# Optimization experiments

Hardware: AMD Instinct MI355X
Metric: run time of the kernel (lower is better)

## Reference

```python
import jax, jax.numpy as jnp
import numpy as np

B, QL, H, HKV, D, MAX_SEQ = 16, 32, 32, 8, 128, 8192
CACHE_LEN = 4064  # tokens already in cache before this step
SCALE = 1.0 / np.sqrt(D).astype(np.float32)


def setup_inputs() -> dict:
    key = jax.random.key(0)
    ks = jax.random.split(key, 5)
    return {
        "q": jax.random.normal(ks[0], (B, QL, H, D), jnp.float32),
        "k": jax.random.normal(ks[1], (B, QL, HKV, D), jnp.float32),
        "v": jax.random.normal(ks[2], (B, QL, HKV, D), jnp.float32),
        "k_cache": jax.random.normal(ks[3], (B, MAX_SEQ, HKV, D), jnp.float32),
        "v_cache": jax.random.normal(ks[4], (B, MAX_SEQ, HKV, D), jnp.float32),
        "cache_seq_len": CACHE_LEN,
    }


def _attention(q, k_full, v_full):
    # q: [B, QL, H, D]; k_full/v_full: [B, KV, HKV, D]. GQA via head grouping
    # (equivalent to repeat_interleave on kv heads, without materializing it).
    rep = H // HKV
    kv_len = k_full.shape[1]
    qr = q.reshape(B, QL, HKV, rep, D)
    scores = jnp.einsum('bqhrd,bkhd->bhrqk', qr, k_full) * SCALE
    # causal mask: position j masked for query i when j > kv_len - QL + i
    mask = jnp.triu(jnp.ones((QL, kv_len), bool), k=kv_len - QL + 1)
    scores = jnp.where(mask, -jnp.inf, scores)
    weights = jax.nn.softmax(scores, axis=-1)
    out = jnp.einsum('bhrqk,bkhd->bqhrd', weights, v_full)
    return out.reshape(B, QL, H, D)


def reference(q, k, v, k_cache, v_cache, cache_seq_len):
    new_len = cache_seq_len + QL  # python int -> static slice
    k_cache = jax.lax.dynamic_update_slice(k_cache, k, (0, cache_seq_len, 0, 0))
    v_cache = jax.lax.dynamic_update_slice(v_cache, v, (0, cache_seq_len, 0, 0))
    k_full = k_cache[:, :new_len]
    v_full = v_cache[:, :new_len]
    return _attention(q, k_full, v_full)
```

## Files before the change

### kernel.cpp

```cpp
#include <hip/hip_runtime.h>

typedef unsigned short ushort_t;
typedef ushort_t ushort8 __attribute__((ext_vector_type(8)));
typedef __bf16 bf16x8 __attribute__((ext_vector_type(8)));
typedef float f32x4 __attribute__((ext_vector_type(4)));
typedef float f32x16 __attribute__((ext_vector_type(16)));
typedef unsigned uint4v __attribute__((ext_vector_type(4)));

#define B_      16
#define QL_     32
#define H_      32
#define HKV_    8
#define D_      128
#define MAXSEQ_ 8192
#define REP_    4
#define ROWS_   128
#define KT_     64
#define NT_     256
#define KS_LD   136
#define VT_LD   72
#define NROWS_TOT (B_*HKV_*ROWS_)
#define KVSTRIDE (HKV_*D_)

__device__ __forceinline__ unsigned pkbf(float lo, float hi2) {
  unsigned a  = (unsigned)__builtin_bit_cast(ushort_t, (__bf16)lo);
  unsigned b2 = (unsigned)__builtin_bit_cast(ushort_t, (__bf16)hi2);
  return a | (b2 << 16);
}

template<int NSPLIT, bool DIRECT>
__global__ __launch_bounds__(NT_, 2)
void fa_main(const float* __restrict__ qg, const float* __restrict__ kg,
             const float* __restrict__ vg, const float* __restrict__ kcg,
             const float* __restrict__ vcg, const int* __restrict__ cslp,
             float* __restrict__ outg, float* __restrict__ opart,
             float* __restrict__ mpart, float* __restrict__ lpart)
{
  __shared__ __align__(16) ushort_t Ks[2][KT_ * KS_LD];
  __shared__ __align__(16) ushort_t Vt[2][D_ * VT_LD];

  const int t    = threadIdx.x;
  const int s    = (int)blockIdx.x % NSPLIT;
  const int bh   = (int)blockIdx.x / NSPLIT;
  const int b    = bh / HKV_;
  const int h    = bh % HKV_;
  const int cl   = cslp[0];
  const int kvlen = cl + QL_;
  const int ntiles = (kvlen + KT_ - 1) / KT_;
  const int tps  = (ntiles + NSPLIT - 1) / NSPLIT;
  const int tt0  = s * tps;
  const int tt1  = min(ntiles, tt0 + tps);

  const int lane = t & 63;
  const int w    = t >> 6;
  const int qcol = lane & 31;
  const int hi   = lane >> 5;

  const float qscale = 0.088388347648318447f * 1.4426950408889634f;
  bf16x8 aQ[8];
  {
    const float* src = qg + (((size_t)b*QL_ + qcol)*H_ + h*REP_ + w)*D_ + hi*8;
    #pragma unroll
    for (int ks = 0; ks < 8; ++ks) {
      f32x4 v0 = *(const f32x4*)(src + ks*16);
      f32x4 v1 = *(const f32x4*)(src + ks*16 + 4);
      bf16x8 u;
      u[0]=(__bf16)(v0[0]*qscale); u[1]=(__bf16)(v0[1]*qscale);
      u[2]=(__bf16)(v0[2]*qscale); u[3]=(__bf16)(v0[3]*qscale);
      u[4]=(__bf16)(v1[0]*qscale); u[5]=(__bf16)(v1[1]*qscale);
      u[6]=(__bf16)(v1[2]*qscale); u[7]=(__bf16)(v1[3]*qscale);
      aQ[ks] = u;
    }
  }

  f32x16 oacc[4];
  #pragma unroll
  for (int db = 0; db < 4; ++db)
    #pragma unroll
    for (int r = 0; r < 16; ++r) oacc[db][r] = 0.f;
  float m_run = -INFINITY;
  float l_run = 0.f;

  const int k_kl = t >> 2;
  const int k_d0 = (t & 3) * 32;
  const int v_k2 = (t & 31) * 2;
  const int v_d0 = (t >> 5) * 16;

  const float* kc_base = kcg + (size_t)b*MAXSEQ_*KVSTRIDE + h*D_ + k_d0;
  const float* kn_base = kg  + (size_t)b*QL_*KVSTRIDE    + h*D_ + k_d0;
  const float* vc_base = vcg + (size_t)b*MAXSEQ_*KVSTRIDE + h*D_ + v_d0;
  const float* vn_base = vg  + (size_t)b*QL_*KVSTRIDE    + h*D_ + v_d0;

  f32x4 kr[8], vr[8];

  auto issue = [&](int tt) {
    const int p0 = tt * KT_;
    {
      int p = p0 + k_kl; if (p > kvlen - 1) p = kvlen - 1;
      const float* src = (p < cl) ? kc_base + (size_t)p*KVSTRIDE
                                  : kn_base + (size_t)(p - cl)*KVSTRIDE;
      #pragma unroll
      for (int j = 0; j < 8; ++j) kr[j] = *(const f32x4*)(src + 4*j);
    }
    #pragma unroll
    for (int kk = 0; kk < 2; ++kk) {
      int p = p0 + v_k2 + kk; if (p > kvlen - 1) p = kvlen - 1;
      const float* src = (p < cl) ? vc_base + (size_t)p*KVSTRIDE
                                  : vn_base + (size_t)(p - cl)*KVSTRIDE;
      #pragma unroll
      for (int j = 0; j < 4; ++j) vr[kk*4 + j] = *(const f32x4*)(src + 4*j);
    }
  };

  auto commit = [&](int bufi) {
    #pragma unroll
    for (int c2 = 0; c2 < 4; ++c2) {
      ushort8 u;
      #pragma unroll
      for (int e = 0; e < 4; ++e) {
        u[e]   = __builtin_bit_cast(ushort_t, (__bf16)kr[c2*2][e]);
        u[4+e] = __builtin_bit_cast(ushort_t, (__bf16)kr[c2*2+1][e]);
      }
      *(ushort8*)&Ks[bufi][k_kl*KS_LD + k_d0 + c2*8] = u;
    }
    #pragma unroll
    for (int dj = 0; dj < 16; ++dj) {
      const unsigned pr = pkbf(vr[dj>>2][dj&3], vr[4 + (dj>>2)][dj&3]);
      *(unsigned*)&Vt[bufi][(v_d0 + dj)*VT_LD + v_k2] = pr;
    }
  };

  if (tt0 < tt1) { issue(tt0); commit(0); }
  __syncthreads();

  for (int tt = tt0; tt < tt1; ++tt) {
    const int  cur     = (tt - tt0) & 1;
    const bool hasNext = (tt + 1 < tt1);
    if (hasNext) issue(tt + 1);

    const int p0 = tt * KT_;

    f32x16 sacc[2];
    __builtin_amdgcn_s_setprio(1);
    #pragma unroll
    for (int kg = 0; kg < 2; ++kg) {
      #pragma unroll
      for (int r = 0; r < 16; ++r) sacc[kg][r] = 0.f;
      #pragma unroll
      for (int ks = 0; ks < 8; ++ks) {
        bf16x8 ak = __builtin_bit_cast(bf16x8,
            *(const ushort8*)&Ks[cur][(kg*32 + qcol)*KS_LD + ks*16 + hi*8]);
        sacc[kg] = __builtin_amdgcn_mfma_f32_32x32x16_bf16(ak, aQ[ks], sacc[kg], 0, 0, 0);
      }
    }
    __builtin_amdgcn_s_setprio(0);

    if (p0 + KT_ - 1 > cl) {
      #pragma unroll
      for (int kg = 0; kg < 2; ++kg)
        #pragma unroll
        for (int r = 0; r < 16; ++r) {
          const int key = p0 + kg*32 + (r&3) + 8*(r>>2) + 4*hi;
          if (key > cl + qcol) sacc[kg][r] = -INFINITY;
        }
    }

    float tm = -INFINITY;
    #pragma unroll
    for (int kg = 0; kg < 2; ++kg)
      #pragma unroll
      for (int r = 0; r < 16; ++r) tm = fmaxf(tm, sacc[kg][r]);
    tm = fmaxf(tm, __shfl_xor(tm, 32, 64));

    if (__any(tm > m_run + 11.5f)) {
      const float mn    = fmaxf(m_run, tm);
      const float alpha = exp2f(m_run - mn);
      m_run = mn;
      l_run *= alpha;
      #pragma unroll
      for (int r = 0; r < 16; ++r) {
        const int rq = (r&3) + 8*(r>>2) + 4*hi;
        const float ar = __shfl(alpha, rq, 64);
        #pragma unroll
        for (int db = 0; db < 4; ++db) oacc[db][r] *= ar;
      }
    }

    float rs = 0.f;
    #pragma unroll
    for (int kg = 0; kg < 2; ++kg)
      #pragma unroll
      for (int r = 0; r < 16; ++r) {
        const float e = exp2f(sacc[kg][r] - m_run);
        sacc[kg][r] = e;
        rs += e;
      }
    rs += __shfl_xor(rs, 32, 64);
    l_run += rs;

    #pragma unroll
    for (int kg = 0; kg < 2; ++kg) {
      #pragma unroll
      for (int hl = 0; hl < 2; ++hl) {
        const int rb = hl * 8;
        unsigned a0 = pkbf(sacc[kg][rb+0], sacc[kg][rb+1]);
        unsigned b0 = pkbf(sacc[kg][rb+4], sacc[kg][rb+5]);
        unsigned a1 = pkbf(sacc[kg][rb+2], sacc[kg][rb+3]);
        unsigned b1 = pkbf(sacc[kg][rb+6], sacc[kg][rb+7]);
        asm volatile("v_permlane32_swap_b32 %0, %1" : "+v"(a0), "+v"(b0));
        asm volatile("v_permlane32_swap_b32 %0, %1" : "+v"(a1), "+v"(b1));
        uint4v wv; wv[0] = a0; wv[1] = a1; wv[2] = b0; wv[3] = b1;
        const bf16x8 ap = __builtin_bit_cast(bf16x8, wv);
        const int kbase = kg*32 + hl*16;
        __builtin_amdgcn_s_setprio(1);
        #pragma unroll
        for (int db = 0; db < 4; ++db) {
          bf16x8 bv = __builtin_bit_cast(bf16x8,
              *(const ushort8*)&Vt[cur][(db*32 + qcol)*VT_LD + kbase + hi*8]);
          oacc[db] = __builtin_amdgcn_mfma_f32_32x32x16_bf16(ap, bv, oacc[db], 0, 0, 0);
        }
        __builtin_amdgcn_s_setprio(0);
      }
    }

    if (hasNext) commit(cur ^ 1);
    __syncthreads();
  }

  const float inv_own = (l_run > 0.f) ? 1.f / l_run : 0.f;
  if constexpr (DIRECT) {
    #pragma unroll
    for (int r = 0; r < 16; ++r) {
      const int rq = (r&3) + 8*(r>>2) + 4*hi;
      const float inv = __shfl(inv_own, rq, 64);
      float* dst = outg + (((size_t)b*QL_ + rq)*H_ + h*REP_ + w)*D_ + qcol;
      #pragma unroll
      for (int db = 0; db < 4; ++db) dst[db*32] = oacc[db][r] * inv;
    }
  } else {
    const int R0 = bh * ROWS_ + w * 32;
    #pragma unroll
    for (int r = 0; r < 16; ++r) {
      const int rq = (r&3) + 8*(r>>2) + 4*hi;
      float* dst = opart + ((size_t)s*NROWS_TOT + R0 + rq)*D_ + qcol;
      #pragma unroll
      for (int db = 0; db < 4; ++db) dst[db*32] = oacc[db][r];
    }
    if (lane < 32) {
      mpart[s*NROWS_TOT + R0 + lane] = m_run;
      lpart[s*NROWS_TOT + R0 + lane] = l_run;
    }
  }
}

template<int NS>
__global__ void fa_combine(const float* __restrict__ opart,
                           const float* __restrict__ mpart,
                           const float* __restrict__ lpart,
                           float* __restrict__ outg)
{
  const int idx = (int)blockIdx.x * 256 + (int)threadIdx.x;
  const int R = idx >> 7;
  const int d = idx & 127;
  float mm = -INFINITY;
  #pragma unroll
  for (int si = 0; si < NS; ++si) mm = fmaxf(mm, mpart[si*NROWS_TOT + R]);
  float L = 0.f, o = 0.f;
  #pragma unroll
  for (int si = 0; si < NS; ++si) {
    const float ms = mpart[si*NROWS_TOT + R];
    const float wgt = (ms == -INFINITY) ? 0.f : exp2f(ms - mm);
    L += lpart[si*NROWS_TOT + R] * wgt;
    o += opart[((size_t)si*NROWS_TOT + R)*D_ + d] * wgt;
  }
  const float res = (L > 0.f) ? o / L : 0.f;
  const int b   = R >> 10;
  const int h   = (R >> 7) & 7;
  const int row = R & 127;
  outg[(((size_t)b*QL_ + (row & 31))*H_ + h*REP_ + (row >> 5))*D_ + d] = res;
}

extern "C" void kernel_launch(void* const* d_in, const int* in_sizes, int n_in,
                              void* d_out, int out_size, void* d_ws, size_t ws_size,
                              hipStream_t stream)
{
  const float* qg  = (const float*)d_in[0];
  const float* kg  = (const float*)d_in[1];
  const float* vg  = (const float*)d_in[2];
  const float* kcg = (const float*)d_in[3];
  const float* vcg = (const float*)d_in[4];
  const int*   csl = (const int*)d_in[5];
  float* outg = (float*)d_out;

  const size_t need4 = (size_t)4 * NROWS_TOT * (D_ + 2) * sizeof(float);
  const size_t need2 = (size_t)2 * NROWS_TOT * (D_ + 2) * sizeof(float);
  if (ws_size >= need4) {
    float* opart = (float*)d_ws;
    float* mpart = opart + (size_t)4 * NROWS_TOT * D_;
    float* lpart = mpart + 4 * NROWS_TOT;
    hipLaunchKernelGGL((fa_main<4, false>), dim3(4 * B_ * HKV_), dim3(NT_), 0, stream,
                       qg, kg, vg, kcg, vcg, csl, nullptr, opart, mpart, lpart);
    hipLaunchKernelGGL((fa_combine<4>), dim3(NROWS_TOT * D_ / 256), dim3(256), 0, stream,
                       opart, mpart, lpart, outg);
  } else if (ws_size >= need2) {
    float* opart = (float*)d_ws;
    float* mpart = opart + (size_t)2 * NROWS_TOT * D_;
    float* lpart = mpart + 2 * NROWS_TOT;
    hipLaunchKernelGGL((fa_main<2, false>), dim3(2 * B_ * HKV_), dim3(NT_), 0, stream,
                       qg, kg, vg, kcg, vcg, csl, nullptr, opart, mpart, lpart);
    hipLaunchKernelGGL((fa_combine<2>), dim3(NROWS_TOT * D_ / 256), dim3(256), 0, stream,
                       opart, mpart, lpart, outg);
  } else {
    hipLaunchKernelGGL((fa_main<1, true>), dim3(B_ * HKV_), dim3(NT_), 0, stream,
                       qg, kg, vg, kcg, vcg, csl, outg, nullptr, nullptr, nullptr);
  }
}
```

Measured before the change: 130.1 us.

## Fuse split-KV combine into main kernel via last-block atomic counter

Removes the separate combine kernel. Each split block writes its partials, then increments a per-(batch,head) atomic counter, and the last arriving block merges all splits and writes the output with vectorized loads and stores. It also remaps block indices so that consecutive blocks with the same batch share the same KV head, which may improve L2 locality of K/V reads. The cost is a memset launch for the counters, threadfences, and a serialized tail merge done by one block per group.

```diff
diff --git a/kernel.cpp b/kernel.cpp
--- a/kernel.cpp
+++ b/kernel.cpp
@@ -34,16 +34,29 @@
              const float* __restrict__ vg, const float* __restrict__ kcg,
              const float* __restrict__ vcg, const int* __restrict__ cslp,
              float* __restrict__ outg, float* __restrict__ opart,
-             float* __restrict__ mpart, float* __restrict__ lpart)
+             float* __restrict__ mpart, float* __restrict__ lpart,
+             int* __restrict__ ctrs)
 {
   __shared__ __align__(16) ushort_t Ks[2][KT_ * KS_LD];
   __shared__ __align__(16) ushort_t Vt[2][D_ * VT_LD];
-
-  const int t    = threadIdx.x;
-  const int s    = (int)blockIdx.x % NSPLIT;
-  const int bh   = (int)blockIdx.x / NSPLIT;
-  const int b    = bh / HKV_;
-  const int h    = bh % HKV_;
+  __shared__ int lastFlag;
+
+  const int t = threadIdx.x;
+  int b, h, s;
+  if constexpr (NSPLIT == 4) {
+    const int nid = (int)blockIdx.x;
+    const int g   = ((nid >> 6) << 3) | (nid & 7);
+    h = (nid >> 3) & 7;
+    b = g >> 2;
+    s = g & 3;
+  } else {
+    s = (int)blockIdx.x % NSPLIT;
+    const int bh0 = (int)blockIdx.x / NSPLIT;
+    b = bh0 / HKV_;
+    h = bh0 % HKV_;
+  }
+  const int bh = b * HKV_ + h;
+
   const int cl   = cslp[0];
   const int kvlen = cl + QL_;
   const int ntiles = (kvlen + KT_ - 1) / KT_;
@@ -143,33 +156,33 @@
     f32x16 sacc[2];
     __builtin_amdgcn_s_setprio(1);
     #pragma unroll
-    for (int kg = 0; kg < 2; ++kg) {
-      #pragma unroll
-      for (int r = 0; r < 16; ++r) sacc[kg][r] = 0.f;
+    for (int kg2 = 0; kg2 < 2; ++kg2) {
+      #pragma unroll
+      for (int r = 0; r < 16; ++r) sacc[kg2][r] = 0.f;
       #pragma unroll
       for (int ks = 0; ks < 8; ++ks) {
         bf16x8 ak = __builtin_bit_cast(bf16x8,
-            *(const ushort8*)&Ks[cur][(kg*32 + qcol)*KS_LD + ks*16 + hi*8]);
-        sacc[kg] = __builtin_amdgcn_mfma_f32_32x32x16_bf16(ak, aQ[ks], sacc[kg], 0, 0, 0);
+            *(const ushort8*)&Ks[cur][(kg2*32 + qcol)*KS_LD + ks*16 + hi*8]);
+        sacc[kg2] = __builtin_amdgcn_mfma_f32_32x32x16_bf16(ak, aQ[ks], sacc[kg2], 0, 0, 0);
       }
     }
     __builtin_amdgcn_s_setprio(0);
 
     if (p0 + KT_ - 1 > cl) {
       #pragma unroll
-      for (int kg = 0; kg < 2; ++kg)
+      for (int kg2 = 0; kg2 < 2; ++kg2)
         #pragma unroll
         for (int r = 0; r < 16; ++r) {
-          const int key = p0 + kg*32 + (r&3) + 8*(r>>2) + 4*hi;
-          if (key > cl + qcol) sacc[kg][r] = -INFINITY;
+          const int key = p0 + kg2*32 + (r&3) + 8*(r>>2) + 4*hi;
+          if (key > cl + qcol) sacc[kg2][r] = -INFINITY;
         }
     }
 
     float tm = -INFINITY;
     #pragma unroll
-    for (int kg = 0; kg < 2; ++kg)
-      #pragma unroll
-      for (int r = 0; r < 16; ++r) tm = fmaxf(tm, sacc[kg][r]);
+    for (int kg2 = 0; kg2 < 2; ++kg2)
+      #pragma unroll
+      for (int r = 0; r < 16; ++r) tm = fmaxf(tm, sacc[kg2][r]);
     tm = fmaxf(tm, __shfl_xor(tm, 32, 64));
 
     if (__any(tm > m_run + 11.5f)) {
@@ -188,30 +201,30 @@
 
     float rs = 0.f;
     #pragma unroll
-    for (int kg = 0; kg < 2; ++kg)
+    for (int kg2 = 0; kg2 < 2; ++kg2)
       #pragma unroll
       for (int r = 0; r < 16; ++r) {
-        const float e = exp2f(sacc[kg][r] - m_run);
-        sacc[kg][r] = e;
+        const float e = exp2f(sacc[kg2][r] - m_run);
+        sacc[kg2][r] = e;
         rs += e;
       }
     rs += __shfl_xor(rs, 32, 64);
     l_run += rs;
 
     #pragma unroll
-    for (int kg = 0; kg < 2; ++kg) {
+    for (int kg2 = 0; kg2 < 2; ++kg2) {
       #pragma unroll
       for (int hl = 0; hl < 2; ++hl) {
         const int rb = hl * 8;
-        unsigned a0 = pkbf(sacc[kg][rb+0], sacc[kg][rb+1]);
-        unsigned b0 = pkbf(sacc[kg][rb+4], sacc[kg][rb+5]);
-        unsigned a1 = pkbf(sacc[kg][rb+2], sacc[kg][rb+3]);
-        unsigned b1 = pkbf(sacc[kg][rb+6], sacc[kg][rb+7]);
+        unsigned a0 = pkbf(sacc[kg2][rb+0], sacc[kg2][rb+1]);
+        unsigned b0 = pkbf(sacc[kg2][rb+4], sacc[kg2][rb+5]);
+        unsigned a1 = pkbf(sacc[kg2][rb+2], sacc[kg2][rb+3]);
+        unsigned b1 = pkbf(sacc[kg2][rb+6], sacc[kg2][rb+7]);
         asm volatile("v_permlane32_swap_b32 %0, %1" : "+v"(a0), "+v"(b0));
         asm volatile("v_permlane32_swap_b32 %0, %1" : "+v"(a1), "+v"(b1));
         uint4v wv; wv[0] = a0; wv[1] = a1; wv[2] = b0; wv[3] = b1;
         const bf16x8 ap = __builtin_bit_cast(bf16x8, wv);
-        const int kbase = kg*32 + hl*16;
+        const int kbase = kg2*32 + hl*16;
         __builtin_amdgcn_s_setprio(1);
         #pragma unroll
         for (int db = 0; db < 4; ++db) {
@@ -227,8 +240,8 @@
     __syncthreads();
   }
 
-  const float inv_own = (l_run > 0.f) ? 1.f / l_run : 0.f;
   if constexpr (DIRECT) {
+    const float inv_own = (l_run > 0.f) ? 1.f / l_run : 0.f;
     #pragma unroll
     for (int r = 0; r < 16; ++r) {
       const int rq = (r&3) + 8*(r>>2) + 4*hi;
@@ -237,6 +250,7 @@
       #pragma unroll
       for (int db = 0; db < 4; ++db) dst[db*32] = oacc[db][r] * inv;
     }
+    return;
   } else {
     const int R0 = bh * ROWS_ + w * 32;
     #pragma unroll
@@ -250,34 +264,43 @@
       mpart[s*NROWS_TOT + R0 + lane] = m_run;
       lpart[s*NROWS_TOT + R0 + lane] = l_run;
     }
-  }
-}
-
-template<int NS>
-__global__ void fa_combine(const float* __restrict__ opart,
-                           const float* __restrict__ mpart,
-                           const float* __restrict__ lpart,
-                           float* __restrict__ outg)
-{
-  const int idx = (int)blockIdx.x * 256 + (int)threadIdx.x;
-  const int R = idx >> 7;
-  const int d = idx & 127;
-  float mm = -INFINITY;
-  #pragma unroll
-  for (int si = 0; si < NS; ++si) mm = fmaxf(mm, mpart[si*NROWS_TOT + R]);
-  float L = 0.f, o = 0.f;
-  #pragma unroll
-  for (int si = 0; si < NS; ++si) {
-    const float ms = mpart[si*NROWS_TOT + R];
-    const float wgt = (ms == -INFINITY) ? 0.f : exp2f(ms - mm);
-    L += lpart[si*NROWS_TOT + R] * wgt;
-    o += opart[((size_t)si*NROWS_TOT + R)*D_ + d] * wgt;
-  }
-  const float res = (L > 0.f) ? o / L : 0.f;
-  const int b   = R >> 10;
-  const int h   = (R >> 7) & 7;
-  const int row = R & 127;
-  outg[(((size_t)b*QL_ + (row & 31))*H_ + h*REP_ + (row >> 5))*D_ + d] = res;
+
+    __threadfence();
+    if (t == 0) lastFlag = (atomicAdd(&ctrs[bh], 1) == NSPLIT - 1);
+    __syncthreads();
+    if (!lastFlag) return;
+    __threadfence();
+
+    const int row = t >> 1;
+    const int d0c = (t & 1) * 64;
+    const int Rb  = bh * ROWS_ + row;
+    float ms[NSPLIT], mm = -INFINITY;
+    #pragma unroll
+    for (int si = 0; si < NSPLIT; ++si) {
+      ms[si] = mpart[si*NROWS_TOT + Rb];
+      mm = fmaxf(mm, ms[si]);
+    }
+    float wgt[NSPLIT], L = 0.f;
+    #pragma unroll
+    for (int si = 0; si < NSPLIT; ++si) {
+      wgt[si] = (ms[si] == -INFINITY) ? 0.f : exp2f(ms[si] - mm);
+      L += lpart[si*NROWS_TOT + Rb] * wgt[si];
+    }
+    const float Linv = (L > 0.f) ? 1.f / L : 0.f;
+    float* dst = outg + (((size_t)b*QL_ + (row & 31))*H_ + h*REP_ + (row >> 5))*D_ + d0c;
+    #pragma unroll
+    for (int j = 0; j < 16; ++j) {
+      f32x4 acc = (f32x4){0.f, 0.f, 0.f, 0.f};
+      #pragma unroll
+      for (int si = 0; si < NSPLIT; ++si) {
+        f32x4 v4 = *(const f32x4*)&opart[((size_t)si*NROWS_TOT + Rb)*D_ + d0c + j*4];
+        acc[0] += v4[0]*wgt[si]; acc[1] += v4[1]*wgt[si];
+        acc[2] += v4[2]*wgt[si]; acc[3] += v4[3]*wgt[si];
+      }
+      acc[0] *= Linv; acc[1] *= Linv; acc[2] *= Linv; acc[3] *= Linv;
+      *(f32x4*)&dst[j*4] = acc;
+    }
+  }
 }
 
 extern "C" void kernel_launch(void* const* d_in, const int* in_sizes, int n_in,
@@ -292,26 +315,18 @@
   const int*   csl = (const int*)d_in[5];
   float* outg = (float*)d_out;
 
-  const size_t need4 = (size_t)4 * NROWS_TOT * (D_ + 2) * sizeof(float);
-  const size_t need2 = (size_t)2 * NROWS_TOT * (D_ + 2) * sizeof(float);
+  const size_t need4 = (size_t)4 * NROWS_TOT * (D_ + 2) * sizeof(float)
+                       + (B_*HKV_) * sizeof(int);
   if (ws_size >= need4) {
     float* opart = (float*)d_ws;
     float* mpart = opart + (size_t)4 * NROWS_TOT * D_;
     float* lpart = mpart + 4 * NROWS_TOT;
+    int*   ctrs  = (int*)(lpart + 4 * NROWS_TOT);
+    hipMemsetAsync(ctrs, 0, (B_*HKV_) * sizeof(int), stream);
     hipLaunchKernelGGL((fa_main<4, false>), dim3(4 * B_ * HKV_), dim3(NT_), 0, stream,
-                       qg, kg, vg, kcg, vcg, csl, nullptr, opart, mpart, lpart);
-    hipLaunchKernelGGL((fa_combine<4>), dim3(NROWS_TOT * D_ / 256), dim3(256), 0, stream,
-                       opart, mpart, lpart, outg);
-  } else if (ws_size >= need2) {
-    float* opart = (float*)d_ws;
-    float* mpart = opart + (size_t)2 * NROWS_TOT * D_;
-    float* lpart = mpart + 2 * NROWS_TOT;
-    hipLaunchKernelGGL((fa_main<2, false>), dim3(2 * B_ * HKV_), dim3(NT_), 0, stream,
-                       qg, kg, vg, kcg, vcg, csl, nullptr, opart, mpart, lpart);
-    hipLaunchKernelGGL((fa_combine<2>), dim3(NROWS_TOT * D_ / 256), dim3(256), 0, stream,
-                       opart, mpart, lpart, outg);
+                       qg, kg, vg, kcg, vcg, csl, outg, opart, mpart, lpart, ctrs);
   } else {
     hipLaunchKernelGGL((fa_main<1, true>), dim3(B_ * HKV_), dim3(NT_), 0, stream,
-                       qg, kg, vg, kcg, vcg, csl, outg, nullptr, nullptr, nullptr);
+                       qg, kg, vg, kcg, vcg, csl, outg, nullptr, nullptr, nullptr, nullptr);
   }
 }
```

After: 275.4 us. 2.12x slower.

## Deepen K/V global prefetch to two tiles ahead with alternating register sets

Applied to the files above, without the earlier changes.

The main attention loop now keeps two register buffers of K/V data and issues global loads two tiles ahead instead of one, alternating buffer roles each iteration. This gives the global loads more time in flight behind the QK/PV MFMA work, hiding memory latency better on this bandwidth-bound decode-style attention. In exchange, per-thread register use grows by 64 VGPRs, which may reduce occupancy or cause spills. The unused 2-way split launch path is also removed.

```diff
diff --git a/kernel.cpp b/kernel.cpp
--- a/kernel.cpp
+++ b/kernel.cpp
@@ -91,9 +91,9 @@
   const float* vc_base = vcg + (size_t)b*MAXSEQ_*KVSTRIDE + h*D_ + v_d0;
   const float* vn_base = vg  + (size_t)b*QL_*KVSTRIDE    + h*D_ + v_d0;
 
-  f32x4 kr[8], vr[8];
-
-  auto issue = [&](int tt) {
+  f32x4 kr0[8], vr0[8], kr1[8], vr1[8];
+
+  auto issue = [&](int tt, f32x4 (&kr)[8], f32x4 (&vr)[8]) {
     const int p0 = tt * KT_;
     {
       int p = p0 + k_kl; if (p > kvlen - 1) p = kvlen - 1;
@@ -112,7 +112,7 @@
     }
   };
 
-  auto commit = [&](int bufi) {
+  auto commit = [&](f32x4 (&kr)[8], f32x4 (&vr)[8], int bufi) {
     #pragma unroll
     for (int c2 = 0; c2 < 4; ++c2) {
       ushort8 u;
@@ -130,46 +130,42 @@
     }
   };
 
-  if (tt0 < tt1) { issue(tt0); commit(0); }
-  __syncthreads();
-
-  for (int tt = tt0; tt < tt1; ++tt) {
-    const int  cur     = (tt - tt0) & 1;
-    const bool hasNext = (tt + 1 < tt1);
-    if (hasNext) issue(tt + 1);
+  auto tilestep = [&](int tt, f32x4 (&krI)[8], f32x4 (&vrI)[8],
+                      f32x4 (&krC)[8], f32x4 (&vrC)[8], int cur) {
+    if (tt + 2 < tt1) issue(tt + 2, krI, vrI);
 
     const int p0 = tt * KT_;
 
     f32x16 sacc[2];
     __builtin_amdgcn_s_setprio(1);
     #pragma unroll
-    for (int kg = 0; kg < 2; ++kg) {
-      #pragma unroll
-      for (int r = 0; r < 16; ++r) sacc[kg][r] = 0.f;
+    for (int kg2 = 0; kg2 < 2; ++kg2) {
+      #pragma unroll
+      for (int r = 0; r < 16; ++r) sacc[kg2][r] = 0.f;
       #pragma unroll
       for (int ks = 0; ks < 8; ++ks) {
         bf16x8 ak = __builtin_bit_cast(bf16x8,
-            *(const ushort8*)&Ks[cur][(kg*32 + qcol)*KS_LD + ks*16 + hi*8]);
-        sacc[kg] = __builtin_amdgcn_mfma_f32_32x32x16_bf16(ak, aQ[ks], sacc[kg], 0, 0, 0);
+            *(const ushort8*)&Ks[cur][(kg2*32 + qcol)*KS_LD + ks*16 + hi*8]);
+        sacc[kg2] = __builtin_amdgcn_mfma_f32_32x32x16_bf16(ak, aQ[ks], sacc[kg2], 0, 0, 0);
       }
     }
     __builtin_amdgcn_s_setprio(0);
 
     if (p0 + KT_ - 1 > cl) {
       #pragma unroll
-      for (int kg = 0; kg < 2; ++kg)
+      for (int kg2 = 0; kg2 < 2; ++kg2)
         #pragma unroll
         for (int r = 0; r < 16; ++r) {
-          const int key = p0 + kg*32 + (r&3) + 8*(r>>2) + 4*hi;
-          if (key > cl + qcol) sacc[kg][r] = -INFINITY;
+          const int key = p0 + kg2*32 + (r&3) + 8*(r>>2) + 4*hi;
+          if (key > cl + qcol) sacc[kg2][r] = -INFINITY;
         }
     }
 
     float tm = -INFINITY;
     #pragma unroll
-    for (int kg = 0; kg < 2; ++kg)
-      #pragma unroll
-      for (int r = 0; r < 16; ++r) tm = fmaxf(tm, sacc[kg][r]);
+    for (int kg2 = 0; kg2 < 2; ++kg2)
+      #pragma unroll
+      for (int r = 0; r < 16; ++r) tm = fmaxf(tm, sacc[kg2][r]);
     tm = fmaxf(tm, __shfl_xor(tm, 32, 64));
 
     if (__any(tm > m_run + 11.5f)) {
@@ -188,30 +184,30 @@
 
     float rs = 0.f;
     #pragma unroll
-    for (int kg = 0; kg < 2; ++kg)
+    for (int kg2 = 0; kg2 < 2; ++kg2)
       #pragma unroll
       for (int r = 0; r < 16; ++r) {
-        const float e = exp2f(sacc[kg][r] - m_run);
-        sacc[kg][r] = e;
+        const float e = exp2f(sacc[kg2][r] - m_run);
+        sacc[kg2][r] = e;
         rs += e;
       }
     rs += __shfl_xor(rs, 32, 64);
     l_run += rs;
 
     #pragma unroll
-    for (int kg = 0; kg < 2; ++kg) {
+    for (int kg2 = 0; kg2 < 2; ++kg2) {
       #pragma unroll
       for (int hl = 0; hl < 2; ++hl) {
         const int rb = hl * 8;
-        unsigned a0 = pkbf(sacc[kg][rb+0], sacc[kg][rb+1]);
-        unsigned b0 = pkbf(sacc[kg][rb+4], sacc[kg][rb+5]);
-        unsigned a1 = pkbf(sacc[kg][rb+2], sacc[kg][rb+3]);
-        unsigned b1 = pkbf(sacc[kg][rb+6], sacc[kg][rb+7]);
+        unsigned a0 = pkbf(sacc[kg2][rb+0], sacc[kg2][rb+1]);
+        unsigned b0 = pkbf(sacc[kg2][rb+4], sacc[kg2][rb+5]);
+        unsigned a1 = pkbf(sacc[kg2][rb+2], sacc[kg2][rb+3]);
+        unsigned b1 = pkbf(sacc[kg2][rb+6], sacc[kg2][rb+7]);
         asm volatile("v_permlane32_swap_b32 %0, %1" : "+v"(a0), "+v"(b0));
         asm volatile("v_permlane32_swap_b32 %0, %1" : "+v"(a1), "+v"(b1));
         uint4v wv; wv[0] = a0; wv[1] = a1; wv[2] = b0; wv[3] = b1;
         const bf16x8 ap = __builtin_bit_cast(bf16x8, wv);
-        const int kbase = kg*32 + hl*16;
+        const int kbase = kg2*32 + hl*16;
         __builtin_amdgcn_s_setprio(1);
         #pragma unroll
         for (int db = 0; db < 4; ++db) {
@@ -223,12 +219,23 @@
       }
     }
 
-    if (hasNext) commit(cur ^ 1);
+    if (tt + 1 < tt1) commit(krC, vrC, cur ^ 1);
     __syncthreads();
-  }
-
-  const float inv_own = (l_run > 0.f) ? 1.f / l_run : 0.f;
+  };
+
+  const int n = tt1 - tt0;
+  if (n >= 1) issue(tt0, kr0, vr0);
+  if (n >= 2) issue(tt0 + 1, kr1, vr1);
+  if (n >= 1) commit(kr0, vr0, 0);
+  __syncthreads();
+
+  for (int tt = tt0, i = 0; tt < tt1; ++tt, ++i) {
+    if ((i & 1) == 0) tilestep(tt, kr0, vr0, kr1, vr1, 0);
+    else              tilestep(tt, kr1, vr1, kr0, vr0, 1);
+  }
+
   if constexpr (DIRECT) {
+    const float inv_own = (l_run > 0.f) ? 1.f / l_run : 0.f;
     #pragma unroll
     for (int r = 0; r < 16; ++r) {
       const int rq = (r&3) + 8*(r>>2) + 4*hi;
@@ -293,7 +300,6 @@
   float* outg = (float*)d_out;
 
   const size_t need4 = (size_t)4 * NROWS_TOT * (D_ + 2) * sizeof(float);
-  const size_t need2 = (size_t)2 * NROWS_TOT * (D_ + 2) * sizeof(float);
   if (ws_size >= need4) {
     float* opart = (float*)d_ws;
     float* mpart = opart + (size_t)4 * NROWS_TOT * D_;
@@ -302,14 +308,6 @@
                        qg, kg, vg, kcg, vcg, csl, nullptr, opart, mpart, lpart);
     hipLaunchKernelGGL((fa_combine<4>), dim3(NROWS_TOT * D_ / 256), dim3(256), 0, stream,
                        opart, mpart, lpart, outg);
-  } else if (ws_size >= need2) {
-    float* opart = (float*)d_ws;
-    float* mpart = opart + (size_t)2 * NROWS_TOT * D_;
-    float* lpart = mpart + 2 * NROWS_TOT;
-    hipLaunchKernelGGL((fa_main<2, false>), dim3(2 * B_ * HKV_), dim3(NT_), 0, stream,
-                       qg, kg, vg, kcg, vcg, csl, nullptr, opart, mpart, lpart);
-    hipLaunchKernelGGL((fa_combine<2>), dim3(NROWS_TOT * D_ / 256), dim3(256), 0, stream,
-                       opart, mpart, lpart, outg);
   } else {
     hipLaunchKernelGGL((fa_main<1, true>), dim3(B_ * HKV_), dim3(NT_), 0, stream,
                        qg, kg, vg, kcg, vcg, csl, outg, nullptr, nullptr, nullptr);
```

Result: slower. 371.1 us (+185.2%).
